# Kernel tuning notes

Hardware: AMD Instinct MI355X
Metric: run time of the kernel (lower is better)

Reference implementation:

```python
import jax, jax.numpy as jnp
import numpy as np

KK = 9  # 3x3 kernel points
PAD = 1
EPS = 1e-5


def _conv2d(x, w, b):
    # x: [B,C,H,W], w: [O,I,3,3]
    y = jax.lax.conv_general_dilated(
        x, w, window_strides=(1, 1), padding=((PAD, PAD), (PAD, PAD)),
        dimension_numbers=("NCHW", "OIHW", "NCHW"))
    return y + b[None, :, None, None]


def _bilinear_sample_one(img, py, px):
    # img: [C,H,W]; py, px: [KK,H,W] fractional sample coords
    C, H, W = img.shape
    y0 = jnp.floor(py).astype(jnp.int32)
    x0 = jnp.floor(px).astype(jnp.int32)
    wy = py - y0
    wx = px - x0

    def g(yi, xi):
        ok = ((yi >= 0) & (yi < H) & (xi >= 0) & (xi < W)).astype(img.dtype)
        v = img[:, jnp.clip(yi, 0, H - 1), jnp.clip(xi, 0, W - 1)]  # [C,KK,H,W]
        return v * ok[None]

    v00 = g(y0, x0)
    v01 = g(y0, x0 + 1)
    v10 = g(y0 + 1, x0)
    v11 = g(y0 + 1, x0 + 1)
    return (v00 * (1 - wy) * (1 - wx) + v01 * (1 - wy) * wx
            + v10 * wy * (1 - wx) + v11 * wy * wx)  # [C,KK,H,W]


def setup_inputs() -> dict:
    key = jax.random.key(0)
    ks = jax.random.split(key, 8)
    B, C, H, W = 8, 256, 96, 96
    O = 256
    x = jax.random.normal(ks[0], (B, C, H, W), dtype=jnp.float32)
    # modulated DCNv2 offset/mask conv: 3*KK output channels
    w_off = jax.random.normal(ks[1], (3 * KK, C, 3, 3), dtype=jnp.float32) * 0.01
    b_off = jnp.zeros((3 * KK,), dtype=jnp.float32)
    w_dcn = jax.random.normal(ks[2], (O, C, 3, 3), dtype=jnp.float32) * (1.0 / np.sqrt(C * KK))
    b_dcn = jnp.zeros((O,), dtype=jnp.float32)
    gamma = jnp.ones((O,), dtype=jnp.float32)
    beta = jnp.zeros((O,), dtype=jnp.float32)
    running_mean = jax.random.normal(ks[3], (O,), dtype=jnp.float32) * 0.1
    running_var = jax.random.uniform(ks[4], (O,), dtype=jnp.float32, minval=0.5, maxval=1.5)
    return {"x": x, "w_off": w_off, "b_off": b_off, "w_dcn": w_dcn,
            "b_dcn": b_dcn, "gamma": gamma, "beta": beta,
            "running_mean": running_mean, "running_var": running_var}


def reference(x, w_off, b_off, w_dcn, b_dcn, gamma, beta, running_mean, running_var):
    B, C, H, W = x.shape
    O = w_dcn.shape[0]
    # offsets + modulation masks
    om = _conv2d(x, w_off, b_off)                  # [B, 3*KK, H, W]
    offset = om[:, :2 * KK]
    mask = jax.nn.sigmoid(om[:, 2 * KK:])          # [B, KK, H, W]
    off_y = offset[:, 0::2]                        # [B, KK, H, W]
    off_x = offset[:, 1::2]

    ky, kx = jnp.meshgrid(jnp.arange(3), jnp.arange(3), indexing="ij")
    ky = ky.reshape(KK).astype(x.dtype)
    kx = kx.reshape(KK).astype(x.dtype)
    hh = jnp.arange(H, dtype=x.dtype)
    ww = jnp.arange(W, dtype=x.dtype)
    # fractional sampling coordinates per output pixel per kernel point
    py = off_y + hh[None, None, :, None] + ky[None, :, None, None] - PAD
    px = off_x + ww[None, None, None, :] + kx[None, :, None, None] - PAD

    sampled = jax.vmap(_bilinear_sample_one)(x, py, px)  # [B,C,KK,H,W]
    sampled = sampled * mask[:, None]
    out = jnp.einsum("bckhw,ock->bohw", sampled, w_dcn.reshape(O, C, KK))
    out = out + b_dcn[None, :, None, None]
    # BatchNorm (inference, running stats) + ReLU
    inv = jax.lax.rsqrt(running_var + EPS)
    out = (out - running_mean[None, :, None, None]) * (gamma * inv)[None, :, None, None]
    out = out + beta[None, :, None, None]
    return jax.nn.relu(out)
```

## Files before the change

kernel.cpp:

```cpp
#include <hip/hip_runtime.h>
#include <hip/hip_bf16.h>
#include <hip/hip_fp16.h>
#include <cstdint>
#include <cstddef>

#define H 96
#define W 96
#define HW 9216
#define C 256
#define B 8
#define O 256
#define KK 9
#define EPS 1e-5f

typedef __attribute__((ext_vector_type(8))) short short8;
typedef __attribute__((ext_vector_type(4))) float float4v;
typedef __attribute__((ext_vector_type(2))) float float2v;
typedef unsigned short ushort_t;
typedef unsigned int uint_t;

__global__ __launch_bounds__(256) void transpose_x_k(
    const float* __restrict__ x, ushort_t* __restrict__ xt)
{
    __shared__ float tile[64][65];
    int t = threadIdx.x;
    int p0 = blockIdx.x * 64;
    int c0 = blockIdx.y * 64;
    int b  = blockIdx.z;
    {
        int tx = t & 63, ty = t >> 6;
        const float* xb = x + ((size_t)b * C + c0 + ty) * HW + p0 + tx;
#pragma unroll
        for (int i = 0; i < 64; i += 4)
            tile[ty + i][tx] = xb[(size_t)i * HW];
    }
    __syncthreads();
    {
        int tc = t & 31, tp = t >> 5;
        ushort_t* xtb = xt + ((size_t)b * HW + p0) * C + c0;
#pragma unroll
        for (int i = 0; i < 64; i += 8) {
            int p = tp + i;
            float a  = tile[2 * tc][p];
            float bb = tile[2 * tc + 1][p];
            __hip_bfloat162 h2 = __float22bfloat162_rn(make_float2(a, bb));
            uint_t u;
            __builtin_memcpy(&u, &h2, 4);
            *reinterpret_cast<uint_t*>(&xtb[(size_t)p * C + 2 * tc]) = u;
        }
    }
}

__global__ __launch_bounds__(256) void prep_b_k(
    const float* __restrict__ wd, ushort_t* __restrict__ bp)
{
    int idx = blockIdx.x * 256 + threadIdx.x;
    int kk = idx / (O * C);
    int r = idx - kk * O * C;
    int o = r >> 8, c = r & 255;
    float v = wd[((size_t)o * C + c) * KK + kk];
    __hip_bfloat16 hh = __float2bfloat16(v);
    ushort_t u;
    __builtin_memcpy(&u, &hh, 2);
    bp[idx] = u;
}

__global__ __launch_bounds__(256) void prep_bo_k(
    const float* __restrict__ wo, ushort_t* __restrict__ bo)
{
    int idx = blockIdx.x * 256 + threadIdx.x;
    int n = idx / (KK * C);
    int r = idx - n * KK * C;
    int kk = r >> 8, c = r & 255;
    float v = (n < 27) ? wo[((size_t)n * C + c) * KK + kk] : 0.0f;
    __hip_bfloat16 hh = __float2bfloat16(v);
    ushort_t u;
    __builtin_memcpy(&u, &hh, 2);
    bo[idx] = u;
}

__global__ __launch_bounds__(256) void offset_mfma_k(
    const ushort_t* __restrict__ xt, const ushort_t* __restrict__ bo,
    const float* __restrict__ b_off, float* __restrict__ om)
{
    int t = threadIdx.x;
    int wv = t >> 6, l = t & 63;
    int ln = l & 15, lq = l >> 4;
    int d = blockIdx.x;
    int lb = (d & 7) * 72 + (d >> 3);
    int p0 = lb * 128;
    int b = p0 / HW;
    int rem0w = p0 - b * HW + wv * 32;
    const ushort_t* xtb = xt + (size_t)b * HW * C;

    int hh0[2], ww0[2];
#pragma unroll
    for (int mt = 0; mt < 2; ++mt) {
        int rem = rem0w + mt * 16 + ln;
        hh0[mt] = rem / W;
        ww0[mt] = rem - hh0[mt] * W;
    }

    float4v acc[2][2];
#pragma unroll
    for (int i = 0; i < 2; ++i)
#pragma unroll
        for (int j = 0; j < 2; ++j) acc[i][j] = (float4v){0.f, 0.f, 0.f, 0.f};

#pragma unroll
    for (int kk = 0; kk < KK; ++kk) {
        int dy = kk / 3 - 1, dx = kk % 3 - 1;
        const ushort_t* ap[2];
        uint_t msk[2];
#pragma unroll
        for (int mt = 0; mt < 2; ++mt) {
            int hh = hh0[mt] + dy, ww = ww0[mt] + dx;
            bool ok = (hh >= 0) & (hh < H) & (ww >= 0) & (ww < W);
            msk[mt] = ok ? 0xffffffffu : 0u;
            int hc = min(max(hh, 0), H - 1);
            int wc = min(max(ww, 0), W - 1);
            ap[mt] = xtb + (size_t)(hc * W + wc) * C + lq * 8;
        }
        const ushort_t* bp0 = bo + ((size_t)(0 * 16 + ln) * KK + kk) * C + lq * 8;
        const ushort_t* bp1 = bo + ((size_t)(1 * 16 + ln) * KK + kk) * C + lq * 8;
#pragma unroll
        for (int cc = 0; cc < 8; ++cc) {
            int c0 = cc * 32;
            short8 af[2];
#pragma unroll
            for (int mt = 0; mt < 2; ++mt) {
                uint4 u = *(const uint4*)(ap[mt] + c0);
                u.x &= msk[mt]; u.y &= msk[mt]; u.z &= msk[mt]; u.w &= msk[mt];
                __builtin_memcpy(&af[mt], &u, 16);
            }
            short8 bf0 = *(const short8*)(bp0 + c0);
            short8 bf1 = *(const short8*)(bp1 + c0);
#pragma unroll
            for (int mt = 0; mt < 2; ++mt) {
                acc[mt][0] = __builtin_amdgcn_mfma_f32_16x16x32_bf16(af[mt], bf0, acc[mt][0], 0, 0, 0);
                acc[mt][1] = __builtin_amdgcn_mfma_f32_16x16x32_bf16(af[mt], bf1, acc[mt][1], 0, 0, 0);
            }
        }
    }

    float* omb = om + (size_t)b * 27 * HW + rem0w;
#pragma unroll
    for (int nt = 0; nt < 2; ++nt) {
        int oc = nt * 16 + ln;
        if (oc < 27) {
            float bv = b_off[oc];
            float* po = omb + (size_t)oc * HW + lq * 4;
#pragma unroll
            for (int mt = 0; mt < 2; ++mt) {
                float4 v;
                v.x = acc[mt][nt].x + bv;
                v.y = acc[mt][nt].y + bv;
                v.z = acc[mt][nt].z + bv;
                v.w = acc[mt][nt].w + bv;
                *(float4*)(po + mt * 16) = v;
            }
        }
    }
}

__device__ __forceinline__ float2v up2(uint_t u) {
    float2v r;
    r.x = __uint_as_float(u << 16);
    r.y = __uint_as_float(u & 0xffff0000u);
    return r;
}

__device__ __forceinline__ uint_t packbf2(float a, float b) {
    __hip_bfloat162 h2 = __float22bfloat162_rn(make_float2(a, b));
    uint_t u;
    __builtin_memcpy(&u, &h2, 4);
    return u;
}

__global__ __launch_bounds__(256) void dcn_main_k(
    const ushort_t* __restrict__ xt, const float* __restrict__ om,
    const ushort_t* __restrict__ bp, const float* __restrict__ b_dcn,
    const float* __restrict__ gamma, const float* __restrict__ beta,
    const float* __restrict__ rmean, const float* __restrict__ rvar,
    float* __restrict__ out)
{
    __shared__ uint3    s_rec[64 * KK];
    __shared__ ushort_t s_a[2][4][64][32];

    int t = threadIdx.x;
    int d = blockIdx.x;
    int lb = (d & 7) * 144 + (d >> 3);
    int p0 = lb * 64;
    int b = p0 / HW;
    int rem0 = p0 - b * HW;

    for (int v = t; v < 64 * KK; v += 256) {
        int m = v & 63;
        int k = v >> 6;
        int rem = rem0 + m;
        int h = rem / W;
        int w = rem - h * W;
        const float* omb = om + (size_t)b * 27 * HW + rem;
        float offy = omb[(size_t)(2 * k) * HW];
        float offx = omb[(size_t)(2 * k + 1) * HW];
        float z    = omb[(size_t)(18 + k) * HW];
        float mval = 1.0f / (1.0f + __expf(-z));
        float py = (float)(h + k / 3 - 1) + offy;
        float px = (float)(w + k % 3 - 1) + offx;
        float fy = floorf(py), fx = floorf(px);
        int y0 = (int)fy, x0 = (int)fx;
        float wy = py - fy, wx = px - fx;
        float row0f = (1.0f - wy) * mval * ((y0 >= 0 && y0 < H) ? 1.0f : 0.0f);
        float row1f = wy * mval * ((y0 >= -1 && y0 < H - 1) ? 1.0f : 0.0f);
        int xsel = min(max(x0, 0), W - 2);
        float wxa = (x0 >= 0 && x0 < W) ? (1.0f - wx) : 0.0f;
        float wxb = (x0 >= -1 && x0 < W - 1) ? wx : 0.0f;
        int cx0 = min(max(x0, 0), W - 1);
        int cx1 = min(max(x0 + 1, 0), W - 1);
        float wA = ((cx0 == xsel) ? wxa : 0.0f) + ((cx1 == xsel) ? wxb : 0.0f);
        float wB = ((cx0 == xsel + 1) ? wxa : 0.0f) + ((cx1 == xsel + 1) ? wxb : 0.0f);
        int yc0 = min(max(y0, 0), H - 1);
        int yc1 = min(max(y0 + 1, 0), H - 1);
        uint3 rr;
        rr.x = (uint_t)(yc0 * W + xsel) | ((uint_t)(yc1 * W + xsel) << 16);
        __half2 h01 = __floats2half2_rn(row0f, row1f);
        __half2 hAB = __floats2half2_rn(wA, wB);
        __builtin_memcpy(&rr.y, &h01, 4);
        __builtin_memcpy(&rr.z, &hAB, 4);
        s_rec[v] = rr;
    }

    float4v acc[4][4];
#pragma unroll
    for (int i = 0; i < 4; ++i)
#pragma unroll
        for (int j = 0; j < 4; ++j)
            acc[i][j] = (float4v){0.f, 0.f, 0.f, 0.f};

    const ushort_t* xtb = xt + (size_t)b * HW * C;
    int wv = t >> 6;
    int l  = t & 63;
    int ln = l & 15;
    int lq = l >> 4;
    int sm = t >> 2;
    int sc = (t & 3) * 8;

    __syncthreads();

#define DECREC(rr_, cb_, a0_, a1_, Wt_) do {                                \
        int px0_ = (rr_).x & 0xffff;                                        \
        int px1_ = (rr_).x >> 16;                                           \
        (a0_) = xtb + (size_t)px0_ * C + (cb_) + sc;                        \
        (a1_) = xtb + (size_t)px1_ * C + (cb_) + sc;                        \
        __half2 h01_, hAB_;                                                 \
        __builtin_memcpy(&h01_, &(rr_).y, 4);                               \
        __builtin_memcpy(&hAB_, &(rr_).z, 4);                               \
        float r0_ = __low2float(h01_), r1_ = __high2float(h01_);            \
        float wa_ = __low2float(hAB_), wb_ = __high2float(hAB_);            \
        (Wt_)[0] = r0_ * wa_; (Wt_)[1] = r0_ * wb_;                         \
        (Wt_)[2] = r1_ * wa_; (Wt_)[3] = r1_ * wb_;                         \
    } while (0)

#define COMBINE(L0_, L1_, L2_, L3_, W_, dst_) do {                          \
        uint4 pk_;                                                          \
        float2v r0_ = up2((L0_).x) * (W_)[0] + up2((L1_).x) * (W_)[1]       \
                    + up2((L2_).x) * (W_)[2] + up2((L3_).x) * (W_)[3];      \
        float2v r1_ = up2((L0_).y) * (W_)[0] + up2((L1_).y) * (W_)[1]       \
                    + up2((L2_).y) * (W_)[2] + up2((L3_).y) * (W_)[3];      \
        float2v r2_ = up2((L0_).z) * (W_)[0] + up2((L1_).z) * (W_)[1]       \
                    + up2((L2_).z) * (W_)[2] + up2((L3_).z) * (W_)[3];      \
        float2v r3_ = up2((L0_).w) * (W_)[0] + up2((L1_).w) * (W_)[1]       \
                    + up2((L2_).w) * (W_)[2] + up2((L3_).w) * (W_)[3];      \
        pk_.x = packbf2(r0_.x, r0_.y);                                      \
        pk_.y = packbf2(r1_.x, r1_.y);                                      \
        pk_.z = packbf2(r2_.x, r2_.y);                                      \
        pk_.w = packbf2(r3_.x, r3_.y);                                      \
        *(uint4*)(dst_) = pk_;                                              \
    } while (0)

    {
        uint3 rr = s_rec[sm];
        const ushort_t *a0, *a1;
        float Wt[4];
        DECREC(rr, 0, a0, a1, Wt);
#pragma unroll
        for (int ci = 0; ci < 4; ++ci) {
            uint4 L0 = *(const uint4*)(a0 + ci * 32);
            uint4 L1 = *(const uint4*)(a0 + ci * 32 + C);
            uint4 L2 = *(const uint4*)(a1 + ci * 32);
            uint4 L3 = *(const uint4*)(a1 + ci * 32 + C);
            COMBINE(L0, L1, L2, L3, Wt, &s_a[0][ci][sm][sc]);
        }
    }
    __syncthreads();

    for (int ph = 0; ph < 2 * KK; ++ph) {
        int rb = ph & 1;
        int wb = rb ^ 1;
        bool more = (ph < 2 * KK - 1);
        int tap = ph >> 1, hf = ph & 1;

        const ushort_t* a0n = xtb;
        const ushort_t* a1n = xtb;
        float Wn[4] = {0.f, 0.f, 0.f, 0.f};
        if (more) {
            int np = ph + 1;
            uint3 rr = s_rec[(np >> 1) * 64 + sm];
            DECREC(rr, (np & 1) * 128, a0n, a1n, Wn);
        }

        const ushort_t* bpk = bp + ((size_t)tap * O + wv * 64 + ln) * C + hf * 128 + lq * 8;
        short8 bfr[4], bfrN[4];
#pragma unroll
        for (int nt = 0; nt < 4; ++nt)
            bfr[nt] = *(const short8*)(bpk + (size_t)nt * 16 * C);

#pragma unroll
        for (int ci = 0; ci < 4; ++ci) {
            uint4 L0, L1, L2, L3;
            if (more) {
                L0 = *(const uint4*)(a0n + ci * 32);
                L1 = *(const uint4*)(a0n + ci * 32 + C);
                L2 = *(const uint4*)(a1n + ci * 32);
                L3 = *(const uint4*)(a1n + ci * 32 + C);
            }
            if (ci < 3) {
#pragma unroll
                for (int nt = 0; nt < 4; ++nt)
                    bfrN[nt] = *(const short8*)(bpk + (size_t)nt * 16 * C + (ci + 1) * 32);
            }
            short8 af[4];
#pragma unroll
            for (int mt = 0; mt < 4; ++mt)
                af[mt] = *(const short8*)&s_a[rb][ci][mt * 16 + ln][lq * 8];
#pragma unroll
            for (int mt = 0; mt < 4; ++mt)
#pragma unroll
                for (int nt = 0; nt < 4; ++nt)
                    acc[mt][nt] = __builtin_amdgcn_mfma_f32_16x16x32_bf16(
                        af[mt], bfr[nt], acc[mt][nt], 0, 0, 0);
            if (more)
                COMBINE(L0, L1, L2, L3, Wn, &s_a[wb][ci][sm][sc]);
#pragma unroll
            for (int nt = 0; nt < 4; ++nt)
                bfr[nt] = bfrN[nt];
        }
        __syncthreads();
    }
#undef COMBINE
#undef DECREC

#pragma unroll
    for (int nt = 0; nt < 4; ++nt) {
        int o = wv * 64 + nt * 16 + ln;
        float scale = gamma[o] * rsqrtf(rvar[o] + EPS);
        float shift = (b_dcn[o] - rmean[o]) * scale + beta[o];
        float* po = out + ((size_t)b * O + o) * HW + rem0 + lq * 4;
#pragma unroll
        for (int mt = 0; mt < 4; ++mt) {
            float4 vv;
            vv.x = fmaxf(acc[mt][nt].x * scale + shift, 0.0f);
            vv.y = fmaxf(acc[mt][nt].y * scale + shift, 0.0f);
            vv.z = fmaxf(acc[mt][nt].z * scale + shift, 0.0f);
            vv.w = fmaxf(acc[mt][nt].w * scale + shift, 0.0f);
            *(float4*)(po + mt * 16) = vv;
        }
    }
}

extern "C" void kernel_launch(void* const* d_in, const int* in_sizes, int n_in,
                              void* d_out, int out_size, void* d_ws, size_t ws_size,
                              hipStream_t stream) {
    const float* x     = (const float*)d_in[0];
    const float* w_off = (const float*)d_in[1];
    const float* b_off = (const float*)d_in[2];
    const float* w_dcn = (const float*)d_in[3];
    const float* b_dcn = (const float*)d_in[4];
    const float* gamma = (const float*)d_in[5];
    const float* beta  = (const float*)d_in[6];
    const float* rmean = (const float*)d_in[7];
    const float* rvar  = (const float*)d_in[8];
    float* out = (float*)d_out;

    float*    om  = (float*)d_ws;
    ushort_t* bpw = (ushort_t*)(om + (size_t)B * 27 * HW);
    ushort_t* bow = bpw + (size_t)KK * O * C;
    ushort_t* xtw = bow + (size_t)32 * KK * C;

    hipLaunchKernelGGL(transpose_x_k, dim3(144, 4, 8), dim3(256), 0, stream,
                       x, xtw);
    hipLaunchKernelGGL(prep_b_k, dim3(2304), dim3(256), 0, stream,
                       w_dcn, bpw);
    hipLaunchKernelGGL(prep_bo_k, dim3(288), dim3(256), 0, stream,
                       w_off, bow);
    hipLaunchKernelGGL(offset_mfma_k, dim3(73728 / 128), dim3(256), 0, stream,
                       xtw, bow, b_off, om);
    hipLaunchKernelGGL(dcn_main_k, dim3(73728 / 64), dim3(256), 0, stream,
                       xtw, om, bpw, b_dcn, gamma, beta, rmean, rvar, out);
}
```

Before: 468.1 us.

## Split DCN main kernel across 512 threads with halved per-wave M tile

The main deformable-conv kernel now runs 512 threads per block instead of 256, with each wave covering 32 pixels by 64 output channels instead of 64 by 64. The bilinear gather and combine work is split across twice as many threads, each handling two channel slices. The register double-buffering of B fragments is dropped in favour of per-step loads. The aim is more waves to hide gather and global latency and lower register pressure per thread, at the cost of B weights being loaded twice per block and less MFMA reuse per A fragment.

```diff
diff --git a/kernel.cpp b/kernel.cpp
--- a/kernel.cpp
+++ b/kernel.cpp
@@ -177,7 +177,7 @@
     return u;
 }
 
-__global__ __launch_bounds__(256) void dcn_main_k(
+__global__ __launch_bounds__(512) void dcn_main_k(
     const ushort_t* __restrict__ xt, const float* __restrict__ om,
     const ushort_t* __restrict__ bp, const float* __restrict__ b_dcn,
     const float* __restrict__ gamma, const float* __restrict__ beta,
@@ -194,7 +194,7 @@
     int b = p0 / HW;
     int rem0 = p0 - b * HW;
 
-    for (int v = t; v < 64 * KK; v += 256) {
+    for (int v = t; v < 64 * KK; v += 512) {
         int m = v & 63;
         int k = v >> 6;
         int rem = rem0 + m;
@@ -230,20 +230,23 @@
         s_rec[v] = rr;
     }
 
-    float4v acc[4][4];
-#pragma unroll
-    for (int i = 0; i < 4; ++i)
+    float4v acc[2][4];
+#pragma unroll
+    for (int i = 0; i < 2; ++i)
 #pragma unroll
         for (int j = 0; j < 4; ++j)
             acc[i][j] = (float4v){0.f, 0.f, 0.f, 0.f};
 
     const ushort_t* xtb = xt + (size_t)b * HW * C;
-    int wv = t >> 6;
     int l  = t & 63;
     int ln = l & 15;
     int lq = l >> 4;
-    int sm = t >> 2;
-    int sc = (t & 3) * 8;
+    int nq = (t >> 6) & 3;
+    int mh = t >> 8;
+    int sm = t >> 3;
+    int sc = (t & 7) * 8;
+    int cs0 = (t >> 2) & 1;
+    int sco = (t & 3) * 8;
 
     __syncthreads();
 
@@ -284,12 +287,12 @@
         float Wt[4];
         DECREC(rr, 0, a0, a1, Wt);
 #pragma unroll
-        for (int ci = 0; ci < 4; ++ci) {
-            uint4 L0 = *(const uint4*)(a0 + ci * 32);
-            uint4 L1 = *(const uint4*)(a0 + ci * 32 + C);
-            uint4 L2 = *(const uint4*)(a1 + ci * 32);
-            uint4 L3 = *(const uint4*)(a1 + ci * 32 + C);
-            COMBINE(L0, L1, L2, L3, Wt, &s_a[0][ci][sm][sc]);
+        for (int cis = 0; cis < 2; ++cis) {
+            uint4 L0 = *(const uint4*)(a0 + cis * 64);
+            uint4 L1 = *(const uint4*)(a0 + cis * 64 + C);
+            uint4 L2 = *(const uint4*)(a1 + cis * 64);
+            uint4 L3 = *(const uint4*)(a1 + cis * 64 + C);
+            COMBINE(L0, L1, L2, L3, Wt, &s_a[0][cis * 2 + cs0][sm][sco]);
         }
     }
     __syncthreads();
@@ -309,41 +312,34 @@
             DECREC(rr, (np & 1) * 128, a0n, a1n, Wn);
         }
 
-        const ushort_t* bpk = bp + ((size_t)tap * O + wv * 64 + ln) * C + hf * 128 + lq * 8;
-        short8 bfr[4], bfrN[4];
-#pragma unroll
-        for (int nt = 0; nt < 4; ++nt)
-            bfr[nt] = *(const short8*)(bpk + (size_t)nt * 16 * C);
-
+        const ushort_t* bpk = bp + ((size_t)tap * O + nq * 64 + ln) * C + hf * 128 + lq * 8;
+
+        uint4 L0, L1, L2, L3;
 #pragma unroll
         for (int ci = 0; ci < 4; ++ci) {
-            uint4 L0, L1, L2, L3;
-            if (more) {
-                L0 = *(const uint4*)(a0n + ci * 32);
-                L1 = *(const uint4*)(a0n + ci * 32 + C);
-                L2 = *(const uint4*)(a1n + ci * 32);
-                L3 = *(const uint4*)(a1n + ci * 32 + C);
+            if (more && (ci & 1) == 0) {
+                int cis = ci >> 1;
+                L0 = *(const uint4*)(a0n + cis * 64);
+                L1 = *(const uint4*)(a0n + cis * 64 + C);
+                L2 = *(const uint4*)(a1n + cis * 64);
+                L3 = *(const uint4*)(a1n + cis * 64 + C);
             }
-            if (ci < 3) {
-#pragma unroll
-                for (int nt = 0; nt < 4; ++nt)
-                    bfrN[nt] = *(const short8*)(bpk + (size_t)nt * 16 * C + (ci + 1) * 32);
-            }
-            short8 af[4];
-#pragma unroll
-            for (int mt = 0; mt < 4; ++mt)
-                af[mt] = *(const short8*)&s_a[rb][ci][mt * 16 + ln][lq * 8];
-#pragma unroll
-            for (int mt = 0; mt < 4; ++mt)
+            short8 bfr[4];
+#pragma unroll
+            for (int nt = 0; nt < 4; ++nt)
+                bfr[nt] = *(const short8*)(bpk + (size_t)nt * 16 * C + ci * 32);
+            short8 af[2];
+#pragma unroll
+            for (int mt = 0; mt < 2; ++mt)
+                af[mt] = *(const short8*)&s_a[rb][ci][mh * 32 + mt * 16 + ln][lq * 8];
+#pragma unroll
+            for (int mt = 0; mt < 2; ++mt)
 #pragma unroll
                 for (int nt = 0; nt < 4; ++nt)
                     acc[mt][nt] = __builtin_amdgcn_mfma_f32_16x16x32_bf16(
                         af[mt], bfr[nt], acc[mt][nt], 0, 0, 0);
-            if (more)
-                COMBINE(L0, L1, L2, L3, Wn, &s_a[wb][ci][sm][sc]);
-#pragma unroll
-            for (int nt = 0; nt < 4; ++nt)
-                bfr[nt] = bfrN[nt];
+            if (more && (ci & 1) == 1)
+                COMBINE(L0, L1, L2, L3, Wn, &s_a[wb][(ci >> 1) * 2 + cs0][sm][sco]);
         }
         __syncthreads();
     }
@@ -352,12 +348,12 @@
 
 #pragma unroll
     for (int nt = 0; nt < 4; ++nt) {
-        int o = wv * 64 + nt * 16 + ln;
+        int o = nq * 64 + nt * 16 + ln;
         float scale = gamma[o] * rsqrtf(rvar[o] + EPS);
         float shift = (b_dcn[o] - rmean[o]) * scale + beta[o];
-        float* po = out + ((size_t)b * O + o) * HW + rem0 + lq * 4;
-#pragma unroll
-        for (int mt = 0; mt < 4; ++mt) {
+        float* po = out + ((size_t)b * O + o) * HW + rem0 + mh * 32 + lq * 4;
+#pragma unroll
+        for (int mt = 0; mt < 2; ++mt) {
             float4 vv;
             vv.x = fmaxf(acc[mt][nt].x * scale + shift, 0.0f);
             vv.y = fmaxf(acc[mt][nt].y * scale + shift, 0.0f);
@@ -395,6 +391,6 @@
                        w_off, bow);
     hipLaunchKernelGGL(offset_mfma_k, dim3(73728 / 128), dim3(256), 0, stream,
                        xtw, bow, b_off, om);
-    hipLaunchKernelGGL(dcn_main_k, dim3(73728 / 64), dim3(256), 0, stream,
+    hipLaunchKernelGGL(dcn_main_k, dim3(73728 / 64), dim3(512), 0, stream,
                        xtw, om, bpw, b_dcn, gamma, beta, rmean, rvar, out);
 }
```

Measured after the change: 618.8 us. 32.2% more time.
